# Optimization experiments

Hardware: AMD Instinct MI355X
Metric: run time of the kernel (lower is better)

## Reference

```python
import jax, jax.numpy as jnp
import numpy as np

N = 50000      # nodes
E = 800000     # edges
G = 1024       # graphs in batch
D_IN = 9       # atom feature dim
D = 64         # embedding_size


def _lin(k, fan_in, shape):
    s = 1.0 / np.sqrt(fan_in)
    return jax.random.uniform(k, shape, jnp.float32, -s, s)


def setup_inputs() -> dict:
    key = jax.random.key(0)
    ks = jax.random.split(key, 12)
    x = jax.random.normal(ks[0], (N, D_IN), dtype=jnp.float32)
    edge_index = jax.random.randint(ks[1], (2, E), 0, N, dtype=jnp.int32)
    # node -> graph id, sorted, every graph non-empty
    batch = (jnp.arange(N) * G // N).astype(jnp.int32)
    W0 = _lin(ks[2], D_IN, (D_IN, D)); b0 = _lin(ks[3], D_IN, (D,))
    W1 = _lin(ks[4], D, (D, D));       b1 = _lin(ks[5], D, (D,))
    W2 = _lin(ks[6], D, (D, D));       b2 = _lin(ks[7], D, (D,))
    W3 = _lin(ks[8], D, (D, D));       b3 = _lin(ks[9], D, (D,))
    Wout = _lin(ks[10], 2 * D, (2 * D, 1)); bout = _lin(ks[11], 2 * D, (1,))
    return {"x": x, "edge_index": edge_index, "batch": batch,
            "W0": W0, "b0": b0, "W1": W1, "b1": b1,
            "W2": W2, "b2": b2, "W3": W3, "b3": b3,
            "Wout": Wout, "bout": bout}


def reference(x, edge_index, batch, W0, b0, W1, b1, W2, b2, W3, b3, Wout, bout):
    n = x.shape[0]
    # GCNConv: add self-loops, symmetric normalization D^-1/2 (A+I) D^-1/2
    loops = jnp.arange(n, dtype=edge_index.dtype)
    row = jnp.concatenate([edge_index[0], loops])  # source
    col = jnp.concatenate([edge_index[1], loops])  # destination
    deg = jax.ops.segment_sum(jnp.ones_like(col, dtype=x.dtype), col, num_segments=n)
    dinv = jax.lax.rsqrt(deg)  # deg >= 1 thanks to self-loops
    norm = dinv[row] * dinv[col]  # [E+N]

    def conv(h, W, b):
        h = h @ W                               # [N, D]
        msg = norm[:, None] * h[row]            # [E+N, D]
        return jax.ops.segment_sum(msg, col, num_segments=n) + b

    h = jnp.tanh(conv(x, W0, b0))
    h = jnp.tanh(conv(h, W1, b1))
    h = jnp.tanh(conv(h, W2, b2))
    h = jnp.tanh(conv(h, W3, b3))
    # dropout is identity in eval mode
    gmax = jax.ops.segment_max(h, batch, num_segments=G)                       # [G, D]
    cnt = jax.ops.segment_sum(jnp.ones((n, 1), h.dtype), batch, num_segments=G)
    gmean = jax.ops.segment_sum(h, batch, num_segments=G) / jnp.maximum(cnt, 1.0)
    pooled = jnp.concatenate([gmax, gmean], axis=1)                            # [G, 2D]
    return pooled @ Wout + bout
```

## Files before the change

### kernel.cpp

```cpp
#include <hip/hip_runtime.h>
#include <hip/hip_fp16.h>
#include <math.h>

#define N_NODES 50000
#define N_EDGES 800000
#define N_GRAPHS 1024
#define DIM 64
#define PAD 64
#define ZROW N_NODES

#define BSHIFT 8
#define BDEST 256
#define NB 196
#define CAP_B 6144
#define EPB 4096

typedef int      v4i __attribute__((ext_vector_type(4)));
typedef float    v4f __attribute__((ext_vector_type(4)));
typedef unsigned v2u __attribute__((ext_vector_type(2)));
typedef unsigned v4u __attribute__((ext_vector_type(4)));

__device__ __forceinline__ int4 ntld4i(const int* p) {
    v4i v = __builtin_nontemporal_load((const v4i*)p);
    return make_int4(v[0], v[1], v[2], v[3]);
}
__device__ __forceinline__ void ntst2u(uint2* p, uint2 v) {
    v2u w; w[0] = v.x; w[1] = v.y;
    __builtin_nontemporal_store(w, (v2u*)p);
}
__device__ __forceinline__ void ntst4u(uint4* p, uint4 v) {
    v4u w; w[0] = v.x; w[1] = v.y; w[2] = v.z; w[3] = v.w;
    __builtin_nontemporal_store(w, (v4u*)p);
}
__device__ __forceinline__ void ntst4f(float4* p, float4 v) {
    v4f w; w[0] = v.x; w[1] = v.y; w[2] = v.z; w[3] = v.w;
    __builtin_nontemporal_store(w, (v4f*)p);
}
__device__ __forceinline__ void ntsth(__half* p, __half v) {
    short s = *(short*)&v;
    __builtin_nontemporal_store(s, (short*)p);
}


__global__ void fill_p1(const int* __restrict__ row, const int* __restrict__ col,
                        int* __restrict__ bcnt, unsigned* __restrict__ bbuf) {
    __shared__ int hist[NB];
    __shared__ int base[NB];
    int tid = threadIdx.x;
    if (tid < NB) hist[tid] = 0;
    __syncthreads();

    int e0 = blockIdx.x * EPB;
    int bk[16]; int rk[16]; unsigned pk[16];
#pragma unroll
    for (int i = 0; i < 4; ++i) {
        int e4 = e0 + i * 1024 + tid * 4;
        bool ok = e4 < N_EDGES;
        int4 c = ok ? ntld4i(col + e4) : make_int4(0, 0, 0, 0);
        int4 r = ok ? ntld4i(row + e4) : make_int4(0, 0, 0, 0);
        int cc[4] = {c.x, c.y, c.z, c.w};
        int rr[4] = {r.x, r.y, r.z, r.w};
#pragma unroll
        for (int j = 0; j < 4; ++j) {
            int q = i * 4 + j;
            if (ok) {
                bk[q] = cc[j] >> BSHIFT;
                pk[q] = ((unsigned)rr[j] << BSHIFT) | (unsigned)(cc[j] & (BDEST - 1));
                rk[q] = atomicAdd(&hist[bk[q]], 1);
            } else {
                bk[q] = -1; rk[q] = 0; pk[q] = 0;
            }
        }
    }
    __syncthreads();
    if (tid < NB) base[tid] = atomicAdd(&bcnt[tid], hist[tid]);
    __syncthreads();
#pragma unroll
    for (int q = 0; q < 16; ++q) {
        if (bk[q] >= 0) {
            int pos = base[bk[q]] + rk[q];
            if (pos < CAP_B) bbuf[(size_t)bk[q] * CAP_B + pos] = pk[q];
        }
    }
}


__global__ void fill_p2(const int* __restrict__ bcnt, const unsigned* __restrict__ bbuf,
                        int* __restrict__ ideg, unsigned short* __restrict__ esrc) {
    __shared__ unsigned short srow[BDEST * PAD];
    __shared__ int ldeg[BDEST];
    int tid = threadIdx.x;
    int b = blockIdx.x;
    {
        uint4* s4 = (uint4*)srow;
        for (int i = tid; i < BDEST * PAD / 8; i += 256) s4[i] = make_uint4(0, 0, 0, 0);
        ldeg[tid] = 0;
    }
    __syncthreads();

    int cnt = min(bcnt[b], CAP_B);
    const unsigned* bp = bbuf + (size_t)b * CAP_B;
    for (int e = tid; e < cnt; e += 256) {
        unsigned u = bp[e];
        int local = u & (BDEST - 1);
        int src = (int)(u >> BSHIFT);
        int k = atomicAdd(&ldeg[local], 1);
        if (k < PAD) srow[local * PAD + k] = (unsigned short)src;
    }
    __syncthreads();

    int dest0 = b << BSHIFT;
    {
        int node = dest0 + tid;
        if (node < N_NODES) ideg[node] = ldeg[tid];
    }
    const uint4* s4 = (const uint4*)srow;
#pragma unroll
    for (int i = 0; i < 8; ++i) {
        int idx = tid + 256 * i;
        int local = idx >> 3;
        int node = dest0 + local;
        if (node < N_NODES)
            ntst4u(&((uint4*)(esrc + (size_t)node * PAD))[idx & 7], s4[idx]);
    }
}


__global__ void gemm9(const float* __restrict__ x, const float* __restrict__ W,
                      const int* __restrict__ ideg, __half* __restrict__ th) {
    __shared__ float Wl[9 * DIM];
    int tid = threadIdx.x;
    if (blockIdx.x == 0 && tid < DIM) th[(size_t)ZROW * DIM + tid] = __float2half(0.0f);
    for (int i = tid; i < 9 * DIM; i += 256) Wl[i] = W[i];
    __syncthreads();
    int node = blockIdx.x * 4 + (tid >> 6);
    int d = tid & 63;
    if (node >= N_NODES) return;
    const float* xr = x + (size_t)node * 9;
    float acc = 0.0f;
#pragma unroll
    for (int k = 0; k < 9; ++k) acc += xr[k] * Wl[k * DIM + d];
    float dv = rsqrtf((float)ideg[node] + 1.0f);
    ntsth(&th[(size_t)node * DIM + d], __float2half(dv * acc));
}

__global__ void gemm64(const float* __restrict__ h, const float* __restrict__ W,
                       const int* __restrict__ ideg, uint2* __restrict__ th2) {
    __shared__ float At[64][68];
    __shared__ float Bl[64][68];
    int tid = threadIdx.x;
    int n0 = blockIdx.x * 64;

    {
        const float4* W4 = (const float4*)W;
#pragma unroll
        for (int i = 0; i < 4; ++i) {
            int idx = tid + 256 * i;
            int k = idx >> 4;
            int d4 = idx & 15;
            float4 v = W4[idx];
            *(float4*)&Bl[k][d4 * 4] = v;
        }
    }
    {
        int node = tid >> 2;
        int seg = tid & 3;
        int gn = n0 + node;
        bool ok = gn < N_NODES;
        const float4* h4 = (const float4*)h;
#pragma unroll
        for (int i = 0; i < 4; ++i) {
            int c4 = seg * 4 + i;
            float4 v = ok ? h4[(size_t)gn * 16 + c4] : make_float4(0.f, 0.f, 0.f, 0.f);
            int d = c4 * 4;
            At[d + 0][node] = v.x;
            At[d + 1][node] = v.y;
            At[d + 2][node] = v.z;
            At[d + 3][node] = v.w;
        }
    }
    __syncthreads();

    int ty = tid >> 4;
    int tx = tid & 15;
    float c00 = 0, c01 = 0, c02 = 0, c03 = 0;
    float c10 = 0, c11 = 0, c12 = 0, c13 = 0;
    float c20 = 0, c21 = 0, c22 = 0, c23 = 0;
    float c30 = 0, c31 = 0, c32 = 0, c33 = 0;
#pragma unroll 8
    for (int k = 0; k < 64; ++k) {
        float4 a = *(const float4*)&At[k][ty * 4];
        float4 b = *(const float4*)&Bl[k][tx * 4];
        c00 += a.x * b.x; c01 += a.x * b.y; c02 += a.x * b.z; c03 += a.x * b.w;
        c10 += a.y * b.x; c11 += a.y * b.y; c12 += a.y * b.z; c13 += a.y * b.w;
        c20 += a.z * b.x; c21 += a.z * b.y; c22 += a.z * b.z; c23 += a.z * b.w;
        c30 += a.w * b.x; c31 += a.w * b.y; c32 += a.w * b.z; c33 += a.w * b.w;
    }
    int gn = n0 + ty * 4;
#define STORE_ROW(r, CA, CB, CC, CD)                                          \
    if (gn + r < N_NODES) {                                                   \
        float dv = rsqrtf((float)ideg[gn + r] + 1.0f);                        \
        __half2 p0 = __floats2half2_rn(dv * CA, dv * CB);                     \
        __half2 p1 = __floats2half2_rn(dv * CC, dv * CD);                     \
        uint2 o;                                                              \
        o.x = *(unsigned*)&p0;                                                \
        o.y = *(unsigned*)&p1;                                                \
        ntst2u(&th2[(size_t)(gn + r) * 16 + tx], o);                          \
    }
    STORE_ROW(0, c00, c01, c02, c03)
    STORE_ROW(1, c10, c11, c12, c13)
    STORE_ROW(2, c20, c21, c22, c23)
    STORE_ROW(3, c30, c31, c32, c33)
#undef STORE_ROW
}


__device__ __forceinline__ float4 h4tof4(uint2 v) {
    __half2 a = *reinterpret_cast<const __half2*>(&v.x);
    __half2 c = *reinterpret_cast<const __half2*>(&v.y);
    float2 fa = __half22float2(a);
    float2 fc = __half22float2(c);
    return make_float4(fa.x, fa.y, fc.x, fc.y);
}

__device__ __forceinline__ void add4(float4& a, const float4& r) {
    a.x += r.x; a.y += r.y; a.z += r.z; a.w += r.w;
}

#define ISSUE(R, BI)                                                          \
    {                                                                         \
        uint4 u_ = ep4[BI];                                                   \
        int rem_ = deg - (BI) * 8;                                            \
        unsigned ww_[4] = {u_.x, u_.y, u_.z, u_.w};                           \
        _Pragma("unroll")                                                     \
        for (int j = 0; j < 8; ++j) {                                         \
            int s_ = (j < rem_) ? (int)((ww_[j >> 1] >> ((j & 1) * 16)) & 0xffffu) : ZROW; \
            R[j] = tb[(size_t)s_ * 16];                                       \
        }                                                                     \
    }

#define CONSUME(R)                                                            \
    {                                                                         \
        _Pragma("unroll")                                                     \
        for (int j = 0; j < 8; ++j) {                                         \
            float4 v_ = h4tof4(R[j]);                                         \
            if ((j & 1) == 0) add4(acc0, v_); else add4(acc1, v_);            \
        }                                                                     \
    }

__global__ __launch_bounds__(256, 7)
void gather_tanh(const unsigned short* __restrict__ esrc, const int* __restrict__ ideg,
                 const uint2* __restrict__ th2, const float* __restrict__ b,
                 float4* __restrict__ hout4) {
    int tid = threadIdx.x;
    int wid = tid >> 6;
    int lane = tid & 63;
    int sub = lane & 15;
    int grp = lane >> 4;
    int node = blockIdx.x * 16 + wid * 4 + grp;

    int deg = min(ideg[node], PAD);
    const uint4* ep4 = (const uint4*)(esrc + node * PAD);
    const uint2* tb = th2 + sub;

    float4 acc0 = h4tof4(tb[(size_t)node * 16]);
    float4 acc1 = make_float4(0.f, 0.f, 0.f, 0.f);

    int nb = (deg + 7) >> 3;
    uint2 rA[8], rB[8];
    if (nb > 0) {
        ISSUE(rA, 0)
        int bi = 0;
        while (bi + 2 <= nb) {
            ISSUE(rB, bi + 1)
            CONSUME(rA)
            if (bi + 2 < nb) ISSUE(rA, bi + 2)
            CONSUME(rB)
            bi += 2;
        }
        if (bi < nb) CONSUME(rA)
    }

    float4 acc;
    acc.x = acc0.x + acc1.x;
    acc.y = acc0.y + acc1.y;
    acc.z = acc0.z + acc1.z;
    acc.w = acc0.w + acc1.w;

    float4 bv = ((const float4*)b)[sub];
    float dv = rsqrtf((float)deg + 1.0f);
    float4 res;
    res.x = tanhf(dv * acc.x + bv.x);
    res.y = tanhf(dv * acc.y + bv.y);
    res.z = tanhf(dv * acc.z + bv.z);
    res.w = tanhf(dv * acc.w + bv.w);
    ntst4f(&hout4[(size_t)node * 16 + sub], res);
}


__device__ __forceinline__ int lower_bound(const int* a, int n, int key) {
    int lo = 0, hi = n;
    while (lo < hi) {
        int mid = (lo + hi) >> 1;
        if (a[mid] < key) lo = mid + 1; else hi = mid;
    }
    return lo;
}

__global__ void pool_out(const float* __restrict__ h, const int* __restrict__ batch,
                         const float* __restrict__ Wout, const float* __restrict__ bout,
                         float* __restrict__ out) {
    __shared__ float smax[4][DIM];
    __shared__ float ssum[4][DIM];
    __shared__ int bounds[2];
    int g = blockIdx.x;
    int tid = threadIdx.x, w = tid >> 6, d = tid & 63;
    if (tid == 0) {
        bounds[0] = lower_bound(batch, N_NODES, g);
        bounds[1] = lower_bound(batch, N_NODES, g + 1);
    }
    __syncthreads();
    int start = bounds[0], end = bounds[1];
    float mx = -INFINITY, sum = 0.0f;
    for (int n = start + w; n < end; n += 4) {
        float v = h[(size_t)n * DIM + d];
        mx = fmaxf(mx, v);
        sum += v;
    }
    smax[w][d] = mx;
    ssum[w][d] = sum;
    __syncthreads();
    if (w == 0) {
        mx = fmaxf(fmaxf(smax[0][d], smax[1][d]), fmaxf(smax[2][d], smax[3][d]));
        sum = ssum[0][d] + ssum[1][d] + ssum[2][d] + ssum[3][d];
        float cnt = (float)(end - start);
        float mean = sum / fmaxf(cnt, 1.0f);
        float v = mx * Wout[d] + mean * Wout[DIM + d];
#pragma unroll
        for (int off = 32; off > 0; off >>= 1) v += __shfl_down(v, off, 64);
        if (d == 0) out[g] = v + bout[0];
    }
}


static inline size_t align256(size_t x) { return (x + 255) & ~(size_t)255; }

extern "C" void kernel_launch(void* const* d_in, const int* in_sizes, int n_in,
                              void* d_out, int out_size, void* d_ws, size_t ws_size,
                              hipStream_t stream) {
    const float* x     = (const float*)d_in[0];
    const int*   ei    = (const int*)d_in[1];
    const int*   batch = (const int*)d_in[2];
    const float* W0    = (const float*)d_in[3];
    const float* b0    = (const float*)d_in[4];
    const float* W1    = (const float*)d_in[5];
    const float* b1    = (const float*)d_in[6];
    const float* W2    = (const float*)d_in[7];
    const float* b2    = (const float*)d_in[8];
    const float* W3    = (const float*)d_in[9];
    const float* b3    = (const float*)d_in[10];
    const float* Wout  = (const float*)d_in[11];
    const float* bout  = (const float*)d_in[12];
    float* out = (float*)d_out;

    const int* row = ei;
    const int* col = ei + N_EDGES;

    char* ws = (char*)d_ws;
    size_t off = 0;
    int*            ideg = (int*)(ws + off);            off += align256((size_t)N_NODES * 4);
    unsigned short* esrc = (unsigned short*)(ws + off); off += align256((size_t)N_NODES * PAD * 2);
    __half*         th   = (__half*)(ws + off);         off += align256(((size_t)N_NODES + 1) * DIM * 2);
    float*          hA   = (float*)(ws + off);          off += align256((size_t)N_NODES * DIM * 4);
    unsigned*       bbuf = (unsigned*)(ws + off);       off += align256((size_t)NB * CAP_B * 4);
    int*            bcnt = (int*)(ws + off);            off += align256((size_t)NB * 4);
    (void)ws_size;

    const int wave_blocks = N_NODES / 4;
    const int gath_blocks = N_NODES / 16;
    const int gemm_blocks = (N_NODES + 63) / 64;

    hipMemsetAsync(bcnt, 0, (size_t)NB * 4, stream);
    fill_p1<<<NB, 256, 0, stream>>>(row, col, bcnt, bbuf);
    fill_p2<<<NB, 256, 0, stream>>>(bcnt, bbuf, ideg, esrc);

    gemm9<<<wave_blocks, 256, 0, stream>>>(x, W0, ideg, th);
    gather_tanh<<<gath_blocks, 256, 0, stream>>>(esrc, ideg, (const uint2*)th, b0, (float4*)hA);

    const float* Ws[3] = {W1, W2, W3};
    const float* bs[3] = {b1, b2, b3};
    for (int l = 0; l < 3; ++l) {
        gemm64<<<gemm_blocks, 256, 0, stream>>>(hA, Ws[l], ideg, (uint2*)th);
        gather_tanh<<<gath_blocks, 256, 0, stream>>>(esrc, ideg, (const uint2*)th, bs[l], (float4*)hA);
    }

    pool_out<<<N_GRAPHS, 256, 0, stream>>>(hA, batch, Wout, bout, out);
    (void)out_size; (void)n_in; (void)in_sizes;
}
```

Baseline: 235.0 us.

## Split node features into two 32-column planes so gather reads half rows

Stores the fp16 transformed features and the fp32 activations as two column planes of 32 features each, and has gather blocks each handle one plane for 32 nodes. Each plane is half the size of the full feature matrix, so the random neighbour gathers work over a smaller footprint that may stay in cache better. In exchange, every edge list is read twice (once per plane), grid parallelism changes, and gemm64 and the pooling kernel now read strided plane layouts.

```diff
diff --git a/kernel.cpp b/kernel.cpp
--- a/kernel.cpp
+++ b/kernel.cpp
@@ -8,6 +8,10 @@
 #define DIM 64
 #define PAD 64
 #define ZROW N_NODES
+
+#define PL_H  ((size_t)(N_NODES + 1) * 32)
+#define PL_U2 ((size_t)(N_NODES + 1) * 8)
+#define PLA_F4 ((size_t)N_NODES * 8)
 
 #define BSHIFT 8
 #define BDEST 256
@@ -130,7 +134,8 @@
                       const int* __restrict__ ideg, __half* __restrict__ th) {
     __shared__ float Wl[9 * DIM];
     int tid = threadIdx.x;
-    if (blockIdx.x == 0 && tid < DIM) th[(size_t)ZROW * DIM + tid] = __float2half(0.0f);
+    if (blockIdx.x == 0 && tid < DIM)
+        th[(size_t)(tid >> 5) * PL_H + (size_t)ZROW * 32 + (tid & 31)] = __float2half(0.0f);
     for (int i = tid; i < 9 * DIM; i += 256) Wl[i] = W[i];
     __syncthreads();
     int node = blockIdx.x * 4 + (tid >> 6);
@@ -141,7 +146,7 @@
 #pragma unroll
     for (int k = 0; k < 9; ++k) acc += xr[k] * Wl[k * DIM + d];
     float dv = rsqrtf((float)ideg[node] + 1.0f);
-    ntsth(&th[(size_t)node * DIM + d], __float2half(dv * acc));
+    ntsth(&th[(size_t)(d >> 5) * PL_H + (size_t)node * 32 + (d & 31)], __float2half(dv * acc));
 }
 
 __global__ void gemm64(const float* __restrict__ h, const float* __restrict__ W,
@@ -171,7 +176,8 @@
 #pragma unroll
         for (int i = 0; i < 4; ++i) {
             int c4 = seg * 4 + i;
-            float4 v = ok ? h4[(size_t)gn * 16 + c4] : make_float4(0.f, 0.f, 0.f, 0.f);
+            float4 v = ok ? h4[(size_t)(c4 >> 3) * PLA_F4 + (size_t)gn * 8 + (c4 & 7)]
+                          : make_float4(0.f, 0.f, 0.f, 0.f);
             int d = c4 * 4;
             At[d + 0][node] = v.x;
             At[d + 1][node] = v.y;
@@ -197,6 +203,8 @@
         c30 += a.w * b.x; c31 += a.w * b.y; c32 += a.w * b.z; c33 += a.w * b.w;
     }
     int gn = n0 + ty * 4;
+    size_t pbase = (size_t)(tx >> 3) * PL_U2;
+    int txl = tx & 7;
 #define STORE_ROW(r, CA, CB, CC, CD)                                          \
     if (gn + r < N_NODES) {                                                   \
         float dv = rsqrtf((float)ideg[gn + r] + 1.0f);                        \
@@ -205,7 +213,7 @@
         uint2 o;                                                              \
         o.x = *(unsigned*)&p0;                                                \
         o.y = *(unsigned*)&p1;                                                \
-        ntst2u(&th2[(size_t)(gn + r) * 16 + tx], o);                          \
+        ntst2u(&th2[pbase + (size_t)(gn + r) * 8 + txl], o);                  \
     }
     STORE_ROW(0, c00, c01, c02, c03)
     STORE_ROW(1, c10, c11, c12, c13)
@@ -235,7 +243,7 @@
         _Pragma("unroll")                                                     \
         for (int j = 0; j < 8; ++j) {                                         \
             int s_ = (j < rem_) ? (int)((ww_[j >> 1] >> ((j & 1) * 16)) & 0xffffu) : ZROW; \
-            R[j] = tb[(size_t)s_ * 16];                                       \
+            R[j] = tb[(size_t)s_ * 8];                                        \
         }                                                                     \
     }
 
@@ -253,32 +261,35 @@
                  const uint2* __restrict__ th2, const float* __restrict__ b,
                  float4* __restrict__ hout4) {
     int tid = threadIdx.x;
+    int plane = blockIdx.x & 1;
+    int nb0 = (blockIdx.x >> 1) * 32;
     int wid = tid >> 6;
     int lane = tid & 63;
-    int sub = lane & 15;
-    int grp = lane >> 4;
-    int node = blockIdx.x * 16 + wid * 4 + grp;
+    int sub = lane & 7;
+    int grp = lane >> 3;
+    int node = nb0 + wid * 8 + grp;
+    if (node >= N_NODES) return;
 
     int deg = min(ideg[node], PAD);
     const uint4* ep4 = (const uint4*)(esrc + node * PAD);
-    const uint2* tb = th2 + sub;
-
-    float4 acc0 = h4tof4(tb[(size_t)node * 16]);
+    const uint2* tb = th2 + plane * PL_U2 + sub;
+
+    float4 acc0 = h4tof4(tb[(size_t)node * 8]);
     float4 acc1 = make_float4(0.f, 0.f, 0.f, 0.f);
 
-    int nb = (deg + 7) >> 3;
+    int nbt = (deg + 7) >> 3;
     uint2 rA[8], rB[8];
-    if (nb > 0) {
+    if (nbt > 0) {
         ISSUE(rA, 0)
         int bi = 0;
-        while (bi + 2 <= nb) {
+        while (bi + 2 <= nbt) {
             ISSUE(rB, bi + 1)
             CONSUME(rA)
-            if (bi + 2 < nb) ISSUE(rA, bi + 2)
+            if (bi + 2 < nbt) ISSUE(rA, bi + 2)
             CONSUME(rB)
             bi += 2;
         }
-        if (bi < nb) CONSUME(rA)
+        if (bi < nbt) CONSUME(rA)
     }
 
     float4 acc;
@@ -287,14 +298,14 @@
     acc.z = acc0.z + acc1.z;
     acc.w = acc0.w + acc1.w;
 
-    float4 bv = ((const float4*)b)[sub];
+    float4 bv = ((const float4*)b)[plane * 8 + sub];
     float dv = rsqrtf((float)deg + 1.0f);
     float4 res;
     res.x = tanhf(dv * acc.x + bv.x);
     res.y = tanhf(dv * acc.y + bv.y);
     res.z = tanhf(dv * acc.z + bv.z);
     res.w = tanhf(dv * acc.w + bv.w);
-    ntst4f(&hout4[(size_t)node * 16 + sub], res);
+    ntst4f(&hout4[(size_t)plane * PLA_F4 + (size_t)node * 8 + sub], res);
 }
 
 
@@ -321,9 +332,10 @@
     }
     __syncthreads();
     int start = bounds[0], end = bounds[1];
+    const float* hp = h + (size_t)(d >> 5) * (size_t)N_NODES * 32 + (d & 31);
     float mx = -INFINITY, sum = 0.0f;
     for (int n = start + w; n < end; n += 4) {
-        float v = h[(size_t)n * DIM + d];
+        float v = hp[(size_t)n * 32];
         mx = fmaxf(mx, v);
         sum += v;
     }
@@ -370,14 +382,14 @@
     size_t off = 0;
     int*            ideg = (int*)(ws + off);            off += align256((size_t)N_NODES * 4);
     unsigned short* esrc = (unsigned short*)(ws + off); off += align256((size_t)N_NODES * PAD * 2);
-    __half*         th   = (__half*)(ws + off);         off += align256(((size_t)N_NODES + 1) * DIM * 2);
-    float*          hA   = (float*)(ws + off);          off += align256((size_t)N_NODES * DIM * 4);
+    __half*         th   = (__half*)(ws + off);         off += align256(2 * PL_H * 2);
+    float*          hA   = (float*)(ws + off);          off += align256(2 * PLA_F4 * 16);
     unsigned*       bbuf = (unsigned*)(ws + off);       off += align256((size_t)NB * CAP_B * 4);
     int*            bcnt = (int*)(ws + off);            off += align256((size_t)NB * 4);
     (void)ws_size;
 
     const int wave_blocks = N_NODES / 4;
-    const int gath_blocks = N_NODES / 16;
+    const int gath_blocks = 2 * 1563;
     const int gemm_blocks = (N_NODES + 63) / 64;
 
     hipMemsetAsync(bcnt, 0, (size_t)NB * 4, stream);
```

Measured after the change: 244.0 us. +3.8%, slower.

## Split neighbor lists by source half and alternate gather order per block

Applied to the files above, without the earlier changes.

Each node's source list is partitioned into low-half and high-half source IDs, stored from opposite ends of the padded row. Per-node block counts go into a new array, and the zero padding is done at build time, so the per-element remainder check in the gather loop goes away. Odd and even gather blocks walk the two halves in opposite order, so concurrent blocks tend to touch the same half of the feature table, which should improve L2 locality. The cost is extra padding work in fill_p2 and one more index array, and the combined block count is capped at eight, which could drop edges when both halves are heavily padded.

```diff
diff --git a/kernel.cpp b/kernel.cpp
--- a/kernel.cpp
+++ b/kernel.cpp
@@ -8,6 +8,7 @@
 #define DIM 64
 #define PAD 64
 #define ZROW N_NODES
+#define HALF_N 25000
 
 #define BSHIFT 8
 #define BDEST 256
@@ -86,16 +87,15 @@
 
 
 __global__ void fill_p2(const int* __restrict__ bcnt, const unsigned* __restrict__ bbuf,
-                        int* __restrict__ ideg, unsigned short* __restrict__ esrc) {
+                        int* __restrict__ ideg, unsigned short* __restrict__ dpk,
+                        unsigned short* __restrict__ esrc) {
     __shared__ unsigned short srow[BDEST * PAD];
-    __shared__ int ldeg[BDEST];
+    __shared__ int llo[BDEST];
+    __shared__ int lhi[BDEST];
     int tid = threadIdx.x;
     int b = blockIdx.x;
-    {
-        uint4* s4 = (uint4*)srow;
-        for (int i = tid; i < BDEST * PAD / 8; i += 256) s4[i] = make_uint4(0, 0, 0, 0);
-        ldeg[tid] = 0;
-    }
+    llo[tid] = 0;
+    lhi[tid] = 0;
     __syncthreads();
 
     int cnt = min(bcnt[b], CAP_B);
@@ -104,24 +104,40 @@
         unsigned u = bp[e];
         int local = u & (BDEST - 1);
         int src = (int)(u >> BSHIFT);
-        int k = atomicAdd(&ldeg[local], 1);
-        if (k < PAD) srow[local * PAD + k] = (unsigned short)src;
+        if (src < HALF_N) {
+            int k = atomicAdd(&llo[local], 1);
+            if (k < PAD) srow[local * PAD + k] = (unsigned short)src;
+        } else {
+            int k = atomicAdd(&lhi[local], 1);
+            if (k < PAD) srow[local * PAD + (PAD - 1 - k)] = (unsigned short)src;
+        }
     }
     __syncthreads();
 
     int dest0 = b << BSHIFT;
-    {
-        int node = dest0 + tid;
-        if (node < N_NODES) ideg[node] = ldeg[tid];
-    }
+    int node = dest0 + tid;
+    if (node < N_NODES) {
+        int loRaw = llo[tid], hiRaw = lhi[tid];
+        int lo = min(loRaw, PAD), hi = min(hiRaw, PAD);
+        int nbA = (lo + 7) >> 3;
+        int nbB = (hi + 7) >> 3;
+        if (nbB > 8 - nbA) nbB = 8 - nbA;
+        for (int i = lo; i < nbA * 8; ++i) srow[tid * PAD + i] = (unsigned short)ZROW;
+        int hiStart = PAD - nbB * 8;
+        for (int i = hiStart; i < PAD - hi; ++i) srow[tid * PAD + i] = (unsigned short)ZROW;
+        ideg[node] = loRaw + hiRaw;
+        dpk[node] = (unsigned short)(nbA | (nbB << 8));
+    }
+    __syncthreads();
+
     const uint4* s4 = (const uint4*)srow;
 #pragma unroll
     for (int i = 0; i < 8; ++i) {
         int idx = tid + 256 * i;
         int local = idx >> 3;
-        int node = dest0 + local;
-        if (node < N_NODES)
-            ntst4u(&((uint4*)(esrc + (size_t)node * PAD))[idx & 7], s4[idx]);
+        int n2 = dest0 + local;
+        if (n2 < N_NODES)
+            ntst4u(&((uint4*)(esrc + (size_t)n2 * PAD))[idx & 7], s4[idx]);
     }
 }
 
@@ -227,14 +243,15 @@
     a.x += r.x; a.y += r.y; a.z += r.z; a.w += r.w;
 }
 
-#define ISSUE(R, BI)                                                          \
+#define BIDX(K) (((K) < n1) ? (s1 + (K)) : (s2 + (K) - n1))
+
+#define ISSUE(R, K)                                                           \
     {                                                                         \
-        uint4 u_ = ep4[BI];                                                   \
-        int rem_ = deg - (BI) * 8;                                            \
+        uint4 u_ = ep4[BIDX(K)];                                              \
         unsigned ww_[4] = {u_.x, u_.y, u_.z, u_.w};                           \
         _Pragma("unroll")                                                     \
         for (int j = 0; j < 8; ++j) {                                         \
-            int s_ = (j < rem_) ? (int)((ww_[j >> 1] >> ((j & 1) * 16)) & 0xffffu) : ZROW; \
+            int s_ = (int)((ww_[j >> 1] >> ((j & 1) * 16)) & 0xffffu);        \
             R[j] = tb[(size_t)s_ * 16];                                       \
         }                                                                     \
     }
@@ -250,6 +267,7 @@
 
 __global__ __launch_bounds__(256, 7)
 void gather_tanh(const unsigned short* __restrict__ esrc, const int* __restrict__ ideg,
+                 const unsigned short* __restrict__ dpk,
                  const uint2* __restrict__ th2, const float* __restrict__ b,
                  float4* __restrict__ hout4) {
     int tid = threadIdx.x;
@@ -258,27 +276,36 @@
     int sub = lane & 15;
     int grp = lane >> 4;
     int node = blockIdx.x * 16 + wid * 4 + grp;
-
-    int deg = min(ideg[node], PAD);
+    int par = blockIdx.x & 1;
+
+    int deg = ideg[node];
+    unsigned pk = dpk[node];
+    int nbA = pk & 0xff;
+    int nbB = (pk >> 8) & 0xff;
+    int hiS = 8 - nbB;
+    int n1 = par ? nbB : nbA;
+    int s1 = par ? hiS : 0;
+    int s2 = par ? 0 : hiS;
+    int nbt = nbA + nbB;
+
     const uint4* ep4 = (const uint4*)(esrc + node * PAD);
     const uint2* tb = th2 + sub;
 
     float4 acc0 = h4tof4(tb[(size_t)node * 16]);
     float4 acc1 = make_float4(0.f, 0.f, 0.f, 0.f);
 
-    int nb = (deg + 7) >> 3;
     uint2 rA[8], rB[8];
-    if (nb > 0) {
+    if (nbt > 0) {
         ISSUE(rA, 0)
         int bi = 0;
-        while (bi + 2 <= nb) {
+        while (bi + 2 <= nbt) {
             ISSUE(rB, bi + 1)
             CONSUME(rA)
-            if (bi + 2 < nb) ISSUE(rA, bi + 2)
+            if (bi + 2 < nbt) ISSUE(rA, bi + 2)
             CONSUME(rB)
             bi += 2;
         }
-        if (bi < nb) CONSUME(rA)
+        if (bi < nbt) CONSUME(rA)
     }
 
     float4 acc;
@@ -369,6 +396,7 @@
     char* ws = (char*)d_ws;
     size_t off = 0;
     int*            ideg = (int*)(ws + off);            off += align256((size_t)N_NODES * 4);
+    unsigned short* dpk  = (unsigned short*)(ws + off); off += align256((size_t)N_NODES * 2);
     unsigned short* esrc = (unsigned short*)(ws + off); off += align256((size_t)N_NODES * PAD * 2);
     __half*         th   = (__half*)(ws + off);         off += align256(((size_t)N_NODES + 1) * DIM * 2);
     float*          hA   = (float*)(ws + off);          off += align256((size_t)N_NODES * DIM * 4);
@@ -382,16 +410,16 @@
 
     hipMemsetAsync(bcnt, 0, (size_t)NB * 4, stream);
     fill_p1<<<NB, 256, 0, stream>>>(row, col, bcnt, bbuf);
-    fill_p2<<<NB, 256, 0, stream>>>(bcnt, bbuf, ideg, esrc);
+    fill_p2<<<NB, 256, 0, stream>>>(bcnt, bbuf, ideg, dpk, esrc);
 
     gemm9<<<wave_blocks, 256, 0, stream>>>(x, W0, ideg, th);
-    gather_tanh<<<gath_blocks, 256, 0, stream>>>(esrc, ideg, (const uint2*)th, b0, (float4*)hA);
+    gather_tanh<<<gath_blocks, 256, 0, stream>>>(esrc, ideg, dpk, (const uint2*)th, b0, (float4*)hA);
 
     const float* Ws[3] = {W1, W2, W3};
     const float* bs[3] = {b1, b2, b3};
     for (int l = 0; l < 3; ++l) {
         gemm64<<<gemm_blocks, 256, 0, stream>>>(hA, Ws[l], ideg, (uint2*)th);
-        gather_tanh<<<gath_blocks, 256, 0, stream>>>(esrc, ideg, (const uint2*)th, bs[l], (float4*)hA);
+        gather_tanh<<<gath_blocks, 256, 0, stream>>>(esrc, ideg, dpk, (const uint2*)th, bs[l], (float4*)hA);
     }
 
     pool_out<<<N_GRAPHS, 256, 0, stream>>>(hA, batch, Wout, bout, out);
```

New measurement: 245.0 us. 1.04x slower.
